# Optimization experiments

Hardware: AMD Instinct MI355X
Metric: run time of the kernel (lower is better)

The kernel has to match this reference:

```python
import jax, jax.numpy as jnp
import numpy as np

B, N, E, H = 4, 2048, 1024, 16
D = E // H
SCALE = 1.0 / np.sqrt(D).astype(np.float32)


def setup_inputs() -> dict:
    key = jax.random.key(0)
    ks = jax.random.split(key, 8)
    xq = jax.random.normal(ks[0], (B, N, E), jnp.float32)
    xk = jax.random.normal(ks[1], (B, N, E), jnp.float32)
    xv = jax.random.normal(ks[2], (B, N, E), jnp.float32)
    # causal mask: True means 'masked out' (matches masked_fill_ semantics)
    attn_mask = jnp.triu(jnp.ones((N, N), dtype=bool), k=1)[None, None]
    Wq = jax.random.normal(ks[3], (E, E), jnp.float32) / np.sqrt(E)
    Wk = jax.random.normal(ks[4], (E, E), jnp.float32) / np.sqrt(E)
    Wv = jax.random.normal(ks[5], (E, E), jnp.float32) / np.sqrt(E)
    Wo = jax.random.normal(ks[6], (E, E), jnp.float32) / np.sqrt(E)
    bo = jnp.zeros((E,), jnp.float32)
    return {"xq": xq, "xk": xk, "xv": xv, "attn_mask": attn_mask,
            "Wq": Wq, "Wk": Wk, "Wv": Wv, "Wo": Wo, "bo": bo}


def _split_heads(x):
    # [B, N, E] -> [B, H, N, D]
    return x.reshape(B, N, H, D).transpose(0, 2, 1, 3)


def reference(xq, xk, xv, attn_mask, Wq, Wk, Wv, Wo, bo):
    # torch nn.Linear: y = x @ W.T
    q = _split_heads(xq @ Wq.T)
    k = _split_heads(xk @ Wk.T)
    v = _split_heads(xv @ Wv.T)
    scores = SCALE * jnp.einsum('bhqd,bhkd->bhqk', q, k)
    scores = jnp.where(attn_mask, -jnp.inf, scores)
    attn = jax.nn.softmax(scores, axis=-1)
    out = jnp.einsum('bhqk,bhkd->bhqd', attn, v)
    out = out.transpose(0, 2, 1, 3).reshape(B, N, E)  # merge heads
    return out @ Wo.T + bo
```

## Files before the change

### kernel.cpp

```cpp
#include <hip/hip_runtime.h>
#include <hip/hip_bf16.h>
#include <stdint.h>
#include <stddef.h>

#define B_ 4
#define N_ 2048
#define E_ 1024
#define H_ 16
#define D_ 64

using bf16 = __hip_bfloat16;
typedef __bf16 bf16x8 __attribute__((ext_vector_type(8)));
typedef float  f32x4  __attribute__((ext_vector_type(4)));
typedef float  f32x16 __attribute__((ext_vector_type(16)));
typedef unsigned int u32x2 __attribute__((ext_vector_type(2)));

__device__ inline bf16x8 load8(const float* p) {
    f32x4 a = *(const f32x4*)p;
    f32x4 b = *(const f32x4*)(p + 4);
    bf16x8 r;
#pragma unroll
    for (int e = 0; e < 4; e++) { r[e] = (__bf16)a[e]; r[e + 4] = (__bf16)b[e]; }
    return r;
}
__device__ inline void store_elem(float* C, size_t idx, float v) { C[idx] = v; }
__device__ inline void store_elem(bf16* C, size_t idx, float v) {
    C[idx] = __float2bfloat16(v);
}

__device__ inline void async_stage16(const bf16* g, bf16* l) {
    __builtin_amdgcn_global_load_lds(
        (const __attribute__((address_space(1))) uint32_t*)g,
        (__attribute__((address_space(3))) uint32_t*)l, 16, 0, 0);
}
__device__ inline void manual_stage16(const float* g, bf16* l) {
    *(bf16x8*)l = load8(g);
}

__global__ __launch_bounds__(256) void cvt_all(
    const float* __restrict__ w0, const float* __restrict__ w1,
    const float* __restrict__ w2, const float* __restrict__ w3,
    bf16* __restrict__ wd,
    const float* __restrict__ x0, const float* __restrict__ x1,
    const float* __restrict__ x2,
    bf16* __restrict__ xd0, bf16* __restrict__ xd1, bf16* __restrict__ xd2)
{
    int bx = blockIdx.x;
    const float* s; bf16* d;
    if (bx < 2048) {
        const int seg = bx >> 9;
        s = seg == 0 ? w0 : seg == 1 ? w1 : seg == 2 ? w2 : w3;
        d = wd + (size_t)seg * (E_ * E_);
        bx &= 511;
    } else {
        bx -= 2048;
        const int seg = bx >> 12;
        s = seg == 0 ? x0 : seg == 1 ? x1 : x2;
        d = seg == 0 ? xd0 : seg == 1 ? xd1 : xd2;
        bx &= 4095;
    }
    const size_t off = ((size_t)bx * 256 + threadIdx.x) * 8;
    *(bf16x8*)&d[off] = load8(s + off);
}

struct GemmB { const void* A[3]; void* C[3]; };

template <typename TA, typename TC>
__global__ __launch_bounds__(256) void gemm_bt(
    GemmB batch, const bf16* __restrict__ Wb, const float* __restrict__ bias)
{
    __shared__ bf16 As[128 * 32];
    __shared__ bf16 Bs[128 * 32];

    const TA*   __restrict__ A = (const TA*)batch.A[blockIdx.z];
    TC*         __restrict__ C = (TC*)batch.C[blockIdx.z];
    const bf16* __restrict__ W = Wb + (size_t)blockIdx.z * (E_ * E_);

    const int tid  = threadIdx.x;
    const int lane = tid & 63;
    const int wave = tid >> 6;
    const int wr   = wave >> 1;
    const int wc   = wave & 1;
    const int r    = lane & 15;
    const int quad = lane >> 4;

    const int m0 = blockIdx.y * 128;
    const int n0 = blockIdx.x * 128;

    const int row0 = tid >> 2,         cc0 = (tid & 3) * 8;
    const int row1 = (tid + 256) >> 2, cc1 = cc0;

    f32x4 acc[4][4];
#pragma unroll
    for (int i = 0; i < 4; i++)
#pragma unroll
        for (int j = 0; j < 4; j++)
            acc[i][j] = {0.0f, 0.0f, 0.0f, 0.0f};

    for (int k0 = 0; k0 < E_; k0 += 32) {
        __syncthreads();
        if constexpr (__is_same(TA, bf16)) {
            async_stage16(&A[(size_t)(m0 + row0) * E_ + k0 + cc0], &As[tid * 8]);
            async_stage16(&A[(size_t)(m0 + row1) * E_ + k0 + cc1], &As[(tid + 256) * 8]);
        } else {
            manual_stage16(&A[(size_t)(m0 + row0) * E_ + k0 + cc0], &As[tid * 8]);
            manual_stage16(&A[(size_t)(m0 + row1) * E_ + k0 + cc1], &As[(tid + 256) * 8]);
        }
        async_stage16(&W[(size_t)(n0 + row0) * E_ + k0 + cc0], &Bs[tid * 8]);
        async_stage16(&W[(size_t)(n0 + row1) * E_ + k0 + cc1], &Bs[(tid + 256) * 8]);
        __syncthreads();

        bf16x8 a[4], b[4];
#pragma unroll
        for (int mt = 0; mt < 4; mt++)
            a[mt] = *(const bf16x8*)&As[(wr * 64 + mt * 16 + r) * 32 + quad * 8];
#pragma unroll
        for (int nt = 0; nt < 4; nt++)
            b[nt] = *(const bf16x8*)&Bs[(wc * 64 + nt * 16 + r) * 32 + quad * 8];
#pragma unroll
        for (int mt = 0; mt < 4; mt++)
#pragma unroll
            for (int nt = 0; nt < 4; nt++)
                acc[mt][nt] = __builtin_amdgcn_mfma_f32_16x16x32_bf16(
                    a[mt], b[nt], acc[mt][nt], 0, 0, 0);
    }

#pragma unroll
    for (int mt = 0; mt < 4; mt++) {
#pragma unroll
        for (int nt = 0; nt < 4; nt++) {
            const int col = n0 + wc * 64 + nt * 16 + r;
            float bv = bias ? bias[col] : 0.0f;
#pragma unroll
            for (int rg = 0; rg < 4; rg++) {
                const int row = m0 + wr * 64 + mt * 16 + quad * 4 + rg;
                store_elem(C, (size_t)row * E_ + col, acc[mt][nt][rg] + bv);
            }
        }
    }
}

__global__ __launch_bounds__(256) void attn_fwd(
    const bf16* __restrict__ q, const bf16* __restrict__ k,
    const bf16* __restrict__ v, bf16* __restrict__ o)
{
    constexpr int LS = 72;
    constexpr float LOG2E = 1.44269504088896340736f;
    __shared__ bf16 Ks[2][64 * LS];
    __shared__ bf16 Vt[2][64 * LS];

    const int tid  = threadIdx.x;
    const int lane = tid & 63;
    const int wave = tid >> 6;
    const int l31  = lane & 31;
    const int hi   = lane >> 5;

    const int l    = blockIdx.x;
    const int xcd  = l & 7;
    const int j    = l >> 3;
    const int bh_hi= j & 7;
    const int a    = (j >> 3) & 3;
    const int slot = j >> 5;
    const int s    = 4 * slot + (a ^ slot);
    const int bh   = (bh_hi << 3) | xcd;
    const int b    = bh >> 4;
    const int h    = bh & 15;

    const size_t basek = (size_t)b * N_ * E_ + (size_t)h * D_;

    const int key0 = tid >> 3;
    const int key1 = key0 + 32;
    const int ck   = (tid & 7) * 8;
    const int kp   = tid & 31;
    const int cv   = (tid >> 5) * 8;

    const int q0 = s * 128;
    const int nt = 2 * s + 2;

    bf16x8 qB[4];
    {
        const size_t qoff =
            ((size_t)b * N_ + q0 + wave * 32 + l31) * E_ + h * D_ + hi * 8;
#pragma unroll
        for (int kc = 0; kc < 4; kc++) {
            qB[kc] = *(const bf16x8*)&q[qoff + kc * 16];
#pragma unroll
            for (int e = 0; e < 8; e++)
                qB[kc][e] = (__bf16)((float)qB[kc][e] * 0.125f);
        }
    }

    float m_i = -1e30f;
    float l_i = 0.0f;
    f32x16 o_acc[2];
#pragma unroll
    for (int rg = 0; rg < 16; rg++) { o_acc[0][rg] = 0.0f; o_acc[1][rg] = 0.0f; }

    bf16x8 kp0, kp1, vp0, vp1;
    kp0 = *(const bf16x8*)&k[basek + (size_t)key0 * E_ + ck];
    kp1 = *(const bf16x8*)&k[basek + (size_t)key1 * E_ + ck];
    vp0 = *(const bf16x8*)&v[basek + (size_t)(2 * kp) * E_ + cv];
    vp1 = *(const bf16x8*)&v[basek + (size_t)(2 * kp + 1) * E_ + cv];
    *(bf16x8*)&Ks[0][key0 * LS + ck] = kp0;
    *(bf16x8*)&Ks[0][key1 * LS + ck] = kp1;
#pragma unroll
    for (int e = 0; e < 8; e++) {
        union { __bf16 hh[2]; uint32_t u; } pk;
        pk.hh[0] = vp0[e]; pk.hh[1] = vp1[e];
        *(uint32_t*)&Vt[0][(cv + e) * LS + 2 * kp] = pk.u;
    }
    {
        const size_t j1 = 64;
        kp0 = *(const bf16x8*)&k[basek + (j1 + key0) * E_ + ck];
        kp1 = *(const bf16x8*)&k[basek + (j1 + key1) * E_ + ck];
        vp0 = *(const bf16x8*)&v[basek + (j1 + 2 * kp) * E_ + cv];
        vp1 = *(const bf16x8*)&v[basek + (j1 + 2 * kp + 1) * E_ + cv];
    }
    __syncthreads();

    for (int t = 0; t < nt; t++) {
        const int cur = t & 1;

        if (t + 1 < nt) {
            *(bf16x8*)&Ks[cur ^ 1][key0 * LS + ck] = kp0;
            *(bf16x8*)&Ks[cur ^ 1][key1 * LS + ck] = kp1;
#pragma unroll
            for (int e = 0; e < 8; e++) {
                union { __bf16 hh[2]; uint32_t u; } pk;
                pk.hh[0] = vp0[e]; pk.hh[1] = vp1[e];
                *(uint32_t*)&Vt[cur ^ 1][(cv + e) * LS + 2 * kp] = pk.u;
            }
        }
        if (t + 2 < nt) {
            const size_t j2 = (size_t)(t + 2) * 64;
            kp0 = *(const bf16x8*)&k[basek + (j2 + key0) * E_ + ck];
            kp1 = *(const bf16x8*)&k[basek + (j2 + key1) * E_ + ck];
            vp0 = *(const bf16x8*)&v[basek + (j2 + 2 * kp) * E_ + cv];
            vp1 = *(const bf16x8*)&v[basek + (j2 + 2 * kp + 1) * E_ + cv];
        }

        f32x16 sf[2];
#pragma unroll
        for (int rg = 0; rg < 16; rg++) { sf[0][rg] = 0.0f; sf[1][rg] = 0.0f; }
#pragma unroll
        for (int kc = 0; kc < 4; kc++) {
            bf16x8 ka0 = *(const bf16x8*)&Ks[cur][l31 * LS + kc * 16 + hi * 8];
            bf16x8 ka1 = *(const bf16x8*)&Ks[cur][(32 + l31) * LS + kc * 16 + hi * 8];
            sf[0] = __builtin_amdgcn_mfma_f32_32x32x16_bf16(ka0, qB[kc], sf[0], 0, 0, 0);
            sf[1] = __builtin_amdgcn_mfma_f32_32x32x16_bf16(ka1, qB[kc], sf[1], 0, 0, 0);
        }

        if (t >= nt - 2) {
            const int qgl   = q0 + wave * 32 + l31;
            const int kbase = t * 64 + 4 * hi;
#pragma unroll
            for (int mt = 0; mt < 2; mt++)
#pragma unroll
                for (int rg = 0; rg < 16; rg++) {
                    const int kgl = kbase + mt * 32 + (rg & 3) + 8 * (rg >> 2);
                    if (kgl > qgl) sf[mt][rg] = -1e30f;
                }
        }

        float mhalf[8];
#pragma unroll
        for (int i = 0; i < 8; i++)
            mhalf[i] = fmaxf(fmaxf(sf[0][2 * i], sf[0][2 * i + 1]),
                             fmaxf(sf[1][2 * i], sf[1][2 * i + 1]));
        float mx = fmaxf(fmaxf(fmaxf(mhalf[0], mhalf[1]), fmaxf(mhalf[2], mhalf[3])),
                         fmaxf(fmaxf(mhalf[4], mhalf[5]), fmaxf(mhalf[6], mhalf[7])));
        mx = fmaxf(mx, __shfl_xor(mx, 32));

        if (!__all(mx <= m_i + 8.0f)) {
            const float m_new = fmaxf(m_i, mx);
            const float al = exp2f((m_i - m_new) * LOG2E);
            l_i *= al;
#pragma unroll
            for (int mo = 0; mo < 2; mo++)
#pragma unroll
                for (int rg = 0; rg < 16; rg++) o_acc[mo][rg] *= al;
            m_i = m_new;
        }

        const float m2 = m_i * LOG2E;
#pragma unroll
        for (int mt = 0; mt < 2; mt++)
#pragma unroll
            for (int rg = 0; rg < 16; rg++)
                sf[mt][rg] = exp2f(__builtin_fmaf(sf[mt][rg], LOG2E, -m2));

        float ls = 0.0f;
#pragma unroll
        for (int mt = 0; mt < 2; mt++) {
            const float a0 = (sf[mt][0] + sf[mt][1]) + (sf[mt][2] + sf[mt][3]);
            const float a1 = (sf[mt][4] + sf[mt][5]) + (sf[mt][6] + sf[mt][7]);
            const float a2 = (sf[mt][8] + sf[mt][9]) + (sf[mt][10] + sf[mt][11]);
            const float a3 = (sf[mt][12] + sf[mt][13]) + (sf[mt][14] + sf[mt][15]);
            ls += (a0 + a1) + (a2 + a3);
        }
        ls += __shfl_xor(ls, 32);
        l_i += ls;

        uint32_t w[2][8];
#pragma unroll
        for (int mt = 0; mt < 2; mt++)
#pragma unroll
            for (int i = 0; i < 8; i++) {
                union { __bf16 hh[2]; uint32_t u; } pk;
                pk.hh[0] = (__bf16)sf[mt][2 * i];
                pk.hh[1] = (__bf16)sf[mt][2 * i + 1];
                w[mt][i] = pk.u;
            }

#pragma unroll
        for (int ks = 0; ks < 4; ks++) {
            const int c  = 4 * (ks & 1);
            const int mt = ks >> 1;
            u32x2 r1 = __builtin_amdgcn_permlane32_swap(
                w[mt][c + 0], w[mt][c + 2], false, false);
            u32x2 r2 = __builtin_amdgcn_permlane32_swap(
                w[mt][c + 1], w[mt][c + 3], false, false);
            union { uint32_t u[4]; bf16x8 v8; } pbu;
            pbu.u[0] = r1[0]; pbu.u[1] = r2[0];
            pbu.u[2] = r1[1]; pbu.u[3] = r2[1];
#pragma unroll
            for (int mo = 0; mo < 2; mo++) {
                bf16x8 va = *(const bf16x8*)
                    &Vt[cur][(mo * 32 + l31) * LS + ks * 16 + hi * 8];
                o_acc[mo] = __builtin_amdgcn_mfma_f32_32x32x16_bf16(
                    va, pbu.v8, o_acc[mo], 0, 0, 0);
            }
        }

        __syncthreads();
    }

    {
        const float invl = 1.0f / l_i;
        const size_t orow =
            ((size_t)b * N_ + q0 + wave * 32 + l31) * E_ + h * D_;
#pragma unroll
        for (int mo = 0; mo < 2; mo++)
#pragma unroll
            for (int g = 0; g < 4; g++) {
                union { __bf16 hh[4]; uint2 u2; } pk;
#pragma unroll
                for (int jj = 0; jj < 4; jj++)
                    pk.hh[jj] = (__bf16)(o_acc[mo][4 * g + jj] * invl);
                *(uint2*)&o[orow + mo * 32 + 8 * g + 4 * hi] = pk.u2;
            }
    }
}

extern "C" void kernel_launch(void* const* d_in, const int* in_sizes, int n_in,
                              void* d_out, int out_size, void* d_ws, size_t ws_size,
                              hipStream_t stream) {
    const float* xq = (const float*)d_in[0];
    const float* xk = (const float*)d_in[1];
    const float* xv = (const float*)d_in[2];
    const float* Wq = (const float*)d_in[4];
    const float* Wk = (const float*)d_in[5];
    const float* Wv = (const float*)d_in[6];
    const float* Wo = (const float*)d_in[7];
    const float* bo = (const float*)d_in[8];
    float* out = (float*)d_out;

    const size_t elems = (size_t)B_ * N_ * E_;
    const size_t wel   = (size_t)E_ * E_;
    bf16* q   = (bf16*)d_ws;
    bf16* kk  = q + elems;
    bf16* vv  = kk + elems;
    bf16* ao  = vv + elems;
    bf16* Wb  = ao + elems;
    bf16* xb0 = Wb + 4 * wel;
    bf16* xb1 = xb0 + elems;
    bf16* xb2 = xb1 + elems;

    const size_t need_big = (7 * elems + 4 * wel) * 2;
    const bool big = ws_size >= need_big;

    dim3 blk(256);
    if (big) {
        cvt_all<<<dim3(14336), blk, 0, stream>>>(
            Wq, Wk, Wv, Wo, Wb, xq, xk, xv, xb0, xb1, xb2);
    } else {
        cvt_all<<<dim3(2048), blk, 0, stream>>>(
            Wq, Wk, Wv, Wo, Wb, nullptr, nullptr, nullptr,
            nullptr, nullptr, nullptr);
    }

    GemmB proj;
    if (big) { proj.A[0] = xb0; proj.A[1] = xb1; proj.A[2] = xb2; }
    else     { proj.A[0] = xq;  proj.A[1] = xk;  proj.A[2] = xv;  }
    proj.C[0] = q; proj.C[1] = kk; proj.C[2] = vv;
    if (big)
        gemm_bt<bf16, bf16><<<dim3(E_ / 128, (B_ * N_) / 128, 3), blk, 0, stream>>>(
            proj, Wb, nullptr);
    else
        gemm_bt<float, bf16><<<dim3(E_ / 128, (B_ * N_) / 128, 3), blk, 0, stream>>>(
            proj, Wb, nullptr);

    attn_fwd<<<dim3(1024), blk, 0, stream>>>(q, kk, vv, ao);

    GemmB fin;
    fin.A[0] = ao; fin.A[1] = ao; fin.A[2] = ao;
    fin.C[0] = out; fin.C[1] = out; fin.C[2] = out;
    gemm_bt<bf16, float><<<dim3(E_ / 128, (B_ * N_) / 128, 1), blk, 0, stream>>>(
        fin, Wb + 3 * wel, bo);
}
```

Measured before the change: 353.9 us.

## Split causal attention along the key dimension and merge partials in a combine kernel

Replaces the single causal attention kernel with a split-KV scheme. The key range of each 128-row query block is cut into chunks of up to 8 tiles, 2560 blocks compute partial outputs plus (max, sum) statistics, and a second kernel merges them. This evens out the uneven causal workload and raises parallelism. In exchange it writes and rereads partial outputs through a scratch buffer and adds a kernel launch. It only applies when the big workspace path is taken.

```diff
diff --git a/kernel.cpp b/kernel.cpp
--- a/kernel.cpp
+++ b/kernel.cpp
@@ -140,6 +140,299 @@
     }
 }
 
+__device__ inline void cid_to_sc(int cid, int& s, int& c) {
+    if (cid < 4)       { s = cid;                 c = 0; }
+    else if (cid < 12) { s = 4 + ((cid - 4) >> 1);  c = (cid - 4) & 1; }
+    else if (cid < 24) { s = 8 + (cid - 12) / 3;    c = (cid - 12) % 3; }
+    else               { s = 12 + ((cid - 24) >> 2); c = (cid - 24) & 3; }
+}
+__device__ inline int cid_base(int s) {
+    return s < 4 ? s : s < 8 ? 4 + 2 * (s - 4)
+         : s < 12 ? 12 + 3 * (s - 8) : 24 + 4 * (s - 12);
+}
+__device__ inline int n_chunks(int s) {
+    return s < 4 ? 1 : s < 8 ? 2 : s < 12 ? 3 : 4;
+}
+
+__global__ __launch_bounds__(256) void attn_part(
+    const bf16* __restrict__ q, const bf16* __restrict__ k,
+    const bf16* __restrict__ v, bf16* __restrict__ op,
+    float2* __restrict__ ml)
+{
+    constexpr int LS = 72;
+    constexpr float LOG2E = 1.44269504088896340736f;
+    __shared__ bf16 Ks[2][64 * LS];
+    __shared__ bf16 Vt[2][64 * LS];
+
+    const int tid  = threadIdx.x;
+    const int lane = tid & 63;
+    const int wave = tid >> 6;
+    const int l31  = lane & 31;
+    const int hi   = lane >> 5;
+
+    const int l     = blockIdx.x;
+    const int xcd   = l & 7;
+    const int idx   = l >> 3;
+    const int bh_hi = idx & 7;
+    const int cid   = idx >> 3;
+    const int bh    = (bh_hi << 3) | xcd;
+    const int b     = bh >> 4;
+    const int h     = bh & 15;
+    int s, c;
+    cid_to_sc(cid, s, c);
+    const int g  = bh * 40 + cid;
+
+    const int q0      = s * 128;
+    const int nt_glob = 2 * s + 2;
+    const int t0      = c * 8;
+    const int t1      = min(t0 + 8, nt_glob);
+
+    const size_t basek = (size_t)b * N_ * E_ + (size_t)h * D_;
+
+    const int key0 = tid >> 3;
+    const int key1 = key0 + 32;
+    const int ck   = (tid & 7) * 8;
+    const int kp   = tid & 31;
+    const int cv   = (tid >> 5) * 8;
+
+    bf16x8 qB[4];
+    {
+        const size_t qoff =
+            ((size_t)b * N_ + q0 + wave * 32 + l31) * E_ + h * D_ + hi * 8;
+#pragma unroll
+        for (int kc = 0; kc < 4; kc++) {
+            qB[kc] = *(const bf16x8*)&q[qoff + kc * 16];
+#pragma unroll
+            for (int e = 0; e < 8; e++)
+                qB[kc][e] = (__bf16)((float)qB[kc][e] * 0.125f);
+        }
+    }
+
+    float m_i = -1e30f;
+    float l_i = 0.0f;
+    f32x16 o_acc[2];
+#pragma unroll
+    for (int rg = 0; rg < 16; rg++) { o_acc[0][rg] = 0.0f; o_acc[1][rg] = 0.0f; }
+
+    bf16x8 kp0, kp1, vp0, vp1;
+    kp0 = *(const bf16x8*)&k[basek + ((size_t)t0 * 64 + key0) * E_ + ck];
+    kp1 = *(const bf16x8*)&k[basek + ((size_t)t0 * 64 + key1) * E_ + ck];
+    vp0 = *(const bf16x8*)&v[basek + ((size_t)t0 * 64 + 2 * kp) * E_ + cv];
+    vp1 = *(const bf16x8*)&v[basek + ((size_t)t0 * 64 + 2 * kp + 1) * E_ + cv];
+    *(bf16x8*)&Ks[0][key0 * LS + ck] = kp0;
+    *(bf16x8*)&Ks[0][key1 * LS + ck] = kp1;
+#pragma unroll
+    for (int e = 0; e < 8; e++) {
+        union { __bf16 hh[2]; uint32_t u; } pk;
+        pk.hh[0] = vp0[e]; pk.hh[1] = vp1[e];
+        *(uint32_t*)&Vt[0][(cv + e) * LS + 2 * kp] = pk.u;
+    }
+    {
+        const size_t j1 = (size_t)(t0 + 1) * 64;
+        kp0 = *(const bf16x8*)&k[basek + (j1 + key0) * E_ + ck];
+        kp1 = *(const bf16x8*)&k[basek + (j1 + key1) * E_ + ck];
+        vp0 = *(const bf16x8*)&v[basek + (j1 + 2 * kp) * E_ + cv];
+        vp1 = *(const bf16x8*)&v[basek + (j1 + 2 * kp + 1) * E_ + cv];
+    }
+    __syncthreads();
+
+    for (int t = t0; t < t1; t++) {
+        const int cur = (t - t0) & 1;
+
+        if (t + 1 < t1) {
+            *(bf16x8*)&Ks[cur ^ 1][key0 * LS + ck] = kp0;
+            *(bf16x8*)&Ks[cur ^ 1][key1 * LS + ck] = kp1;
+#pragma unroll
+            for (int e = 0; e < 8; e++) {
+                union { __bf16 hh[2]; uint32_t u; } pk;
+                pk.hh[0] = vp0[e]; pk.hh[1] = vp1[e];
+                *(uint32_t*)&Vt[cur ^ 1][(cv + e) * LS + 2 * kp] = pk.u;
+            }
+        }
+        if (t + 2 < t1) {
+            const size_t j2 = (size_t)(t + 2) * 64;
+            kp0 = *(const bf16x8*)&k[basek + (j2 + key0) * E_ + ck];
+            kp1 = *(const bf16x8*)&k[basek + (j2 + key1) * E_ + ck];
+            vp0 = *(const bf16x8*)&v[basek + (j2 + 2 * kp) * E_ + cv];
+            vp1 = *(const bf16x8*)&v[basek + (j2 + 2 * kp + 1) * E_ + cv];
+        }
+
+        f32x16 sf[2];
+#pragma unroll
+        for (int rg = 0; rg < 16; rg++) { sf[0][rg] = 0.0f; sf[1][rg] = 0.0f; }
+#pragma unroll
+        for (int kc = 0; kc < 4; kc++) {
+            bf16x8 ka0 = *(const bf16x8*)&Ks[cur][l31 * LS + kc * 16 + hi * 8];
+            bf16x8 ka1 = *(const bf16x8*)&Ks[cur][(32 + l31) * LS + kc * 16 + hi * 8];
+            sf[0] = __builtin_amdgcn_mfma_f32_32x32x16_bf16(ka0, qB[kc], sf[0], 0, 0, 0);
+            sf[1] = __builtin_amdgcn_mfma_f32_32x32x16_bf16(ka1, qB[kc], sf[1], 0, 0, 0);
+        }
+
+        if (t >= nt_glob - 2) {
+            const int qgl   = q0 + wave * 32 + l31;
+            const int kbase = t * 64 + 4 * hi;
+#pragma unroll
+            for (int mt = 0; mt < 2; mt++)
+#pragma unroll
+                for (int rg = 0; rg < 16; rg++) {
+                    const int kgl = kbase + mt * 32 + (rg & 3) + 8 * (rg >> 2);
+                    if (kgl > qgl) sf[mt][rg] = -1e30f;
+                }
+        }
+
+        float mhalf[8];
+#pragma unroll
+        for (int i = 0; i < 8; i++)
+            mhalf[i] = fmaxf(fmaxf(sf[0][2 * i], sf[0][2 * i + 1]),
+                             fmaxf(sf[1][2 * i], sf[1][2 * i + 1]));
+        float mx = fmaxf(fmaxf(fmaxf(mhalf[0], mhalf[1]), fmaxf(mhalf[2], mhalf[3])),
+                         fmaxf(fmaxf(mhalf[4], mhalf[5]), fmaxf(mhalf[6], mhalf[7])));
+        mx = fmaxf(mx, __shfl_xor(mx, 32));
+
+        if (!__all(mx <= m_i + 8.0f)) {
+            const float m_new = fmaxf(m_i, mx);
+            const float al = exp2f((m_i - m_new) * LOG2E);
+            l_i *= al;
+#pragma unroll
+            for (int mo = 0; mo < 2; mo++)
+#pragma unroll
+                for (int rg = 0; rg < 16; rg++) o_acc[mo][rg] *= al;
+            m_i = m_new;
+        }
+
+        const float m2 = m_i * LOG2E;
+#pragma unroll
+        for (int mt = 0; mt < 2; mt++)
+#pragma unroll
+            for (int rg = 0; rg < 16; rg++)
+                sf[mt][rg] = exp2f(__builtin_fmaf(sf[mt][rg], LOG2E, -m2));
+
+        float ls = 0.0f;
+#pragma unroll
+        for (int mt = 0; mt < 2; mt++) {
+            const float a0 = (sf[mt][0] + sf[mt][1]) + (sf[mt][2] + sf[mt][3]);
+            const float a1 = (sf[mt][4] + sf[mt][5]) + (sf[mt][6] + sf[mt][7]);
+            const float a2 = (sf[mt][8] + sf[mt][9]) + (sf[mt][10] + sf[mt][11]);
+            const float a3 = (sf[mt][12] + sf[mt][13]) + (sf[mt][14] + sf[mt][15]);
+            ls += (a0 + a1) + (a2 + a3);
+        }
+        ls += __shfl_xor(ls, 32);
+        l_i += ls;
+
+        uint32_t w[2][8];
+#pragma unroll
+        for (int mt = 0; mt < 2; mt++)
+#pragma unroll
+            for (int i = 0; i < 8; i++) {
+                union { __bf16 hh[2]; uint32_t u; } pk;
+                pk.hh[0] = (__bf16)sf[mt][2 * i];
+                pk.hh[1] = (__bf16)sf[mt][2 * i + 1];
+                w[mt][i] = pk.u;
+            }
+
+#pragma unroll
+        for (int ks = 0; ks < 4; ks++) {
+            const int cc = 4 * (ks & 1);
+            const int mt = ks >> 1;
+            u32x2 r1 = __builtin_amdgcn_permlane32_swap(
+                w[mt][cc + 0], w[mt][cc + 2], false, false);
+            u32x2 r2 = __builtin_amdgcn_permlane32_swap(
+                w[mt][cc + 1], w[mt][cc + 3], false, false);
+            union { uint32_t u[4]; bf16x8 v8; } pbu;
+            pbu.u[0] = r1[0]; pbu.u[1] = r2[0];
+            pbu.u[2] = r1[1]; pbu.u[3] = r2[1];
+#pragma unroll
+            for (int mo = 0; mo < 2; mo++) {
+                bf16x8 va = *(const bf16x8*)
+                    &Vt[cur][(mo * 32 + l31) * LS + ks * 16 + hi * 8];
+                o_acc[mo] = __builtin_amdgcn_mfma_f32_32x32x16_bf16(
+                    va, pbu.v8, o_acc[mo], 0, 0, 0);
+            }
+        }
+
+        __syncthreads();
+    }
+
+    {
+        const int row = wave * 32 + l31;
+        const float invl = 1.0f / l_i;
+        const size_t obase = (size_t)g * 8192 + (size_t)row * 64;
+#pragma unroll
+        for (int mo = 0; mo < 2; mo++)
+#pragma unroll
+            for (int gq = 0; gq < 4; gq++) {
+                union { __bf16 hh[4]; uint2 u2; } pk;
+#pragma unroll
+                for (int jj = 0; jj < 4; jj++)
+                    pk.hh[jj] = (__bf16)(o_acc[mo][4 * gq + jj] * invl);
+                *(uint2*)&op[obase + mo * 32 + 8 * gq + 4 * hi] = pk.u2;
+            }
+        if (hi == 0)
+            ml[((size_t)g << 7) + row] = make_float2(m_i, l_i);
+    }
+}
+
+__global__ __launch_bounds__(256) void attn_comb(
+    const bf16* __restrict__ op, const float2* __restrict__ ml,
+    bf16* __restrict__ o)
+{
+    constexpr float LOG2E = 1.44269504088896340736f;
+    const int bid = blockIdx.x;
+    const int bh  = bid >> 4;
+    const int s   = bid & 15;
+    const int b   = bh >> 4;
+    const int h   = bh & 15;
+    const int gb  = bh * 40 + cid_base(s);
+    const int nc  = n_chunks(s);
+
+    const int tid = threadIdx.x;
+    const int row = tid >> 1;
+    const int dof = (tid & 1) * 32;
+
+    float mv[4], lv[4];
+#pragma unroll
+    for (int c = 0; c < 4; c++)
+        if (c < nc) {
+            float2 t = ml[((size_t)(gb + c) << 7) + row];
+            mv[c] = t.x; lv[c] = t.y;
+        }
+    float M = -1e30f;
+#pragma unroll
+    for (int c = 0; c < 4; c++) if (c < nc) M = fmaxf(M, mv[c]);
+    float wt[4]; float L = 0.0f;
+#pragma unroll
+    for (int c = 0; c < 4; c++)
+        if (c < nc) { wt[c] = lv[c] * exp2f((mv[c] - M) * LOG2E); L += wt[c]; }
+    const float invL = 1.0f / L;
+
+    float acc[32];
+#pragma unroll
+    for (int e = 0; e < 32; e++) acc[e] = 0.0f;
+#pragma unroll
+    for (int c = 0; c < 4; c++)
+        if (c < nc) {
+            const float wc = wt[c];
+            const size_t base = (size_t)(gb + c) * 8192 + (size_t)row * 64 + dof;
+#pragma unroll
+            for (int seg = 0; seg < 4; seg++) {
+                bf16x8 v8 = *(const bf16x8*)&op[base + seg * 8];
+#pragma unroll
+                for (int e = 0; e < 8; e++)
+                    acc[seg * 8 + e] = __builtin_fmaf(wc, (float)v8[e], acc[seg * 8 + e]);
+            }
+        }
+
+    const size_t obase = ((size_t)b * N_ + s * 128 + row) * E_ + h * D_ + dof;
+#pragma unroll
+    for (int seg = 0; seg < 4; seg++) {
+        bf16x8 v8;
+#pragma unroll
+        for (int e = 0; e < 8; e++)
+            v8[e] = (__bf16)(acc[seg * 8 + e] * invL);
+        *(bf16x8*)&o[obase + seg * 8] = v8;
+    }
+}
+
 __global__ __launch_bounds__(256) void attn_fwd(
     const bf16* __restrict__ q, const bf16* __restrict__ k,
     const bf16* __restrict__ v, bf16* __restrict__ o)
@@ -220,7 +513,6 @@
 
     for (int t = 0; t < nt; t++) {
         const int cur = t & 1;
-
         if (t + 1 < nt) {
             *(bf16x8*)&Ks[cur ^ 1][key0 * LS + ck] = kp0;
             *(bf16x8*)&Ks[cur ^ 1][key1 * LS + ck] = kp1;
@@ -314,12 +606,12 @@
 
 #pragma unroll
         for (int ks = 0; ks < 4; ks++) {
-            const int c  = 4 * (ks & 1);
+            const int cc = 4 * (ks & 1);
             const int mt = ks >> 1;
             u32x2 r1 = __builtin_amdgcn_permlane32_swap(
-                w[mt][c + 0], w[mt][c + 2], false, false);
+                w[mt][cc + 0], w[mt][cc + 2], false, false);
             u32x2 r2 = __builtin_amdgcn_permlane32_swap(
-                w[mt][c + 1], w[mt][c + 3], false, false);
+                w[mt][cc + 1], w[mt][cc + 3], false, false);
             union { uint32_t u[4]; bf16x8 v8; } pbu;
             pbu.u[0] = r1[0]; pbu.u[1] = r2[0];
             pbu.u[2] = r1[1]; pbu.u[3] = r2[1];
@@ -400,7 +692,14 @@
         gemm_bt<float, bf16><<<dim3(E_ / 128, (B_ * N_) / 128, 3), blk, 0, stream>>>(
             proj, Wb, nullptr);
 
-    attn_fwd<<<dim3(1024), blk, 0, stream>>>(q, kk, vv, ao);
+    if (big) {
+        bf16*   op = xb0;
+        float2* ml = (float2*)(xb0 + (size_t)2560 * 8192);
+        attn_part<<<dim3(2560), blk, 0, stream>>>(q, kk, vv, op, ml);
+        attn_comb<<<dim3(1024), blk, 0, stream>>>(op, ml, ao);
+    } else {
+        attn_fwd<<<dim3(1024), blk, 0, stream>>>(q, kk, vv, ao);
+    }
 
     GemmB fin;
     fin.A[0] = ao; fin.A[1] = ao; fin.A[2] = ao;
```

Measured after the change: 362.4 us. 2.4% more time.
